# Optimization experiments

Measured on AMD Instinct MI355X. Metric: run time of the kernel, lower is better.

## Reference

```python
import jax, jax.numpy as jnp
import numpy as np

CORR_S = 8        # corr_size
IN_EPS = 1e-5     # torch InstanceNorm2d default eps
L2_EPS = 1e-12    # torch F.normalize default eps


def l2_normalize(x):
    # F.normalize(x, p=2, dim=1)
    n = jnp.sqrt(jnp.sum(x * x, axis=1, keepdims=True))
    return x / jnp.maximum(n, L2_EPS)


def instance_norm(x):
    # InstanceNorm2d(affine=False): per-sample, per-channel over H,W; biased var
    m = jnp.mean(x, axis=(2, 3), keepdims=True)
    v = jnp.var(x, axis=(2, 3), keepdims=True)
    return (x - m) * jax.lax.rsqrt(v + IN_EPS)


def setup_inputs() -> dict:
    key = jax.random.key(0)
    ks = jax.random.split(key, 7)
    B, C, H, W = 16, 256, 96, 96
    fc = 64                      # feat_channel
    p = CORR_S * CORR_S          # 64 correlation channels
    x = jax.random.normal(ks[0], (B, C, H, W), jnp.float32)
    # corr_reduce: Conv1x1(p->fc), IN, ReLU, Conv3x3(fc->fc)
    W1 = jax.random.normal(ks[1], (fc, p), jnp.float32) * 0.05
    b1 = jax.random.normal(ks[2], (fc,), jnp.float32) * 0.05
    W2 = jax.random.normal(ks[3], (fc, fc, 3, 3), jnp.float32) * 0.05
    b2 = jax.random.normal(ks[4], (fc,), jnp.float32) * 0.05
    # feat_adapt: Conv1x1(C+fc=320 -> fc), IN, ReLU
    W3 = jax.random.normal(ks[5], (fc, C + fc), jnp.float32) * 0.05
    b3 = jax.random.normal(ks[6], (fc,), jnp.float32) * 0.05
    return {"x": x, "W1": W1, "b1": b1, "W2": W2, "b2": b2, "W3": W3, "b3": b3}


def reference(x, W1, b1, W2, b2, W3, b3):
    B, C, H, W_ = x.shape
    s = CORR_S
    # AdaptiveAvgPool2d((s,s)): H,W divisible by s -> exact window means
    pooled = x.reshape(B, C, s, H // s, s, W_ // s).mean(axis=(3, 5))  # [B,C,s,s]
    ker = l2_normalize(pooled).reshape(B, C, s * s)  # [B,C,p]
    feat = l2_normalize(x)                            # [B,C,H,W]
    # corr_fun: per-sample 1x1 conv == batched contraction over channels
    corr = jnp.einsum('bcp,bchw->bphw', ker, feat)    # [B,p,H,W]
    # corr_reduce
    h = jnp.einsum('op,bphw->bohw', W1, corr) + b1[None, :, None, None]
    h = jax.nn.relu(instance_norm(h))
    h = jax.lax.conv_general_dilated(
        h, W2, window_strides=(1, 1), padding='SAME',
        dimension_numbers=('NCHW', 'OIHW', 'NCHW')) + b2[None, :, None, None]
    # feat_adapt on cat(x, Red_corr)
    new_feat = jnp.concatenate([x, h], axis=1)        # [B,C+fc,H,W]
    out = jnp.einsum('oc,bchw->bohw', W3, new_feat) + b3[None, :, None, None]
    out = jax.nn.relu(instance_norm(out))
    return out
```

## Files before the change

kernel.cpp:

```cpp
#include <hip/hip_runtime.h>

#define BB 16
#define CC 256
#define HW 9216

typedef short bf16x8 __attribute__((ext_vector_type(8)));
typedef float f32x4 __attribute__((ext_vector_type(4)));

__device__ __forceinline__ unsigned short f2bf(float f) {
  unsigned u = __float_as_uint(f);
  return (unsigned short)((u + 0x7FFFu + ((u >> 16) & 1u)) >> 16);
}
__device__ __forceinline__ float bf2f(unsigned short h) {
  return __uint_as_float(((unsigned)h) << 16);
}

__global__ __launch_bounds__(256) void k_pool(const float* __restrict__ x,
                                              float* __restrict__ pooled) {
  int bc = blockIdx.x;
  const float* plane = x + (size_t)bc * HW;
  __shared__ float rowwin[96][8];
  for (int idx = threadIdx.x; idx < 96 * 8; idx += 256) {
    int y = idx >> 3, wx = idx & 7;
    const float* r = plane + y * 96 + wx * 12;
    float s = 0.f;
#pragma unroll
    for (int i = 0; i < 12; ++i) s += r[i];
    rowwin[y][wx] = s;
  }
  __syncthreads();
  if (threadIdx.x < 64) {
    int wy = threadIdx.x >> 3, wx = threadIdx.x & 7;
    float s = 0.f;
#pragma unroll
    for (int i = 0; i < 12; ++i) s += rowwin[wy * 12 + i][wx];
    pooled[(size_t)bc * 64 + threadIdx.x] = s * (1.0f / 144.0f);
  }
}

__global__ __launch_bounds__(256) void k_invn(const float* __restrict__ pooled,
                                              float* __restrict__ invn) {
  int b = blockIdx.x;
  int p = threadIdx.x & 63, cg = threadIdx.x >> 6;
  const float* pb = pooled + (size_t)b * CC * 64;
  float s = 0.f;
  for (int c = cg; c < CC; c += 4) { float v = pb[c * 64 + p]; s += v * v; }
  __shared__ float sm[4][64];
  sm[cg][p] = s;
  __syncthreads();
  if (threadIdx.x < 64) {
    float tot = sm[0][p] + sm[1][p] + sm[2][p] + sm[3][p];
    invn[b * 64 + p] = 1.0f / fmaxf(sqrtf(tot), 1e-12f);
  }
}

__global__ __launch_bounds__(256) void k_M(const float* __restrict__ pooled,
                                           const float* __restrict__ invn,
                                           const float* __restrict__ W1,
                                           unsigned short* __restrict__ Mbf) {
  int c0 = blockIdx.x * 16, b = blockIdx.y, t = threadIdx.x;
  __shared__ float W1s[64][65];
  __shared__ float kers[16][65];
  __shared__ float invs[64];
  if (t < 64) invs[t] = invn[b * 64 + t];
  for (int i = t; i < 4096; i += 256) W1s[i >> 6][i & 63] = W1[i];
  __syncthreads();
  for (int i = t; i < 1024; i += 256) {
    int c = i >> 6, p = i & 63;
    kers[c][p] = pooled[((size_t)b * CC + c0 + c) * 64 + p] * invs[p];
  }
  __syncthreads();
  int c = t & 15, og = t >> 4;
  float s0 = 0.f, s1 = 0.f, s2 = 0.f, s3 = 0.f;
#pragma unroll
  for (int p = 0; p < 64; ++p) {
    float kv = kers[c][p];
    s0 = fmaf(W1s[og * 4 + 0][p], kv, s0);
    s1 = fmaf(W1s[og * 4 + 1][p], kv, s1);
    s2 = fmaf(W1s[og * 4 + 2][p], kv, s2);
    s3 = fmaf(W1s[og * 4 + 3][p], kv, s3);
  }
  unsigned short* Mb = Mbf + (size_t)b * 64 * 256 + c0 + c;
  Mb[(og * 4 + 0) * 256] = f2bf(s0);
  Mb[(og * 4 + 1) * 256] = f2bf(s1);
  Mb[(og * 4 + 2) * 256] = f2bf(s2);
  Mb[(og * 4 + 3) * 256] = f2bf(s3);
}

__global__ void k_prep(const float* __restrict__ W3, unsigned short* __restrict__ W3bf,
                       const float* __restrict__ W2, unsigned short* __restrict__ W2bf,
                       float* __restrict__ statsbuf) {
  int i = blockIdx.x * 256 + threadIdx.x;
  if (i < 64 * 320) W3bf[i] = f2bf(W3[i]);
  if (i < 9 * 64 * 64) {
    int tap = i >> 12, rem = i & 4095;
    int o = rem >> 6, f = rem & 63;
    W2bf[i] = f2bf(W2[(size_t)(o * 64 + f) * 9 + tap]);
  }
  if (i < 4096) statsbuf[i] = 0.f;
}

__global__ __launch_bounds__(256) void k_trans(const float* __restrict__ x,
                                               unsigned short* __restrict__ xT,
                                               float* __restrict__ ssq) {
  int b = blockIdx.y;
  int px0 = blockIdx.x * 64;
  int t = threadIdx.x;
  int px = t & 63, cg = t >> 6;
  __shared__ unsigned char sm[32768];
  __shared__ float sq[64];
  if (t < 64) sq[t] = 0.f;
  __syncthreads();
  float part = 0.f;
  const float* xb = x + (size_t)b * CC * HW + px0 + px;
#pragma unroll
  for (int kk = 0; kk < 8; ++kk) {
    int c = cg * 64 + kk * 8;
    float v[8];
#pragma unroll
    for (int j = 0; j < 8; ++j) {
      v[j] = xb[(size_t)(c + j) * HW];
      part += v[j] * v[j];
    }
    uint4 pk;
    pk.x = (unsigned)f2bf(v[0]) | ((unsigned)f2bf(v[1]) << 16);
    pk.y = (unsigned)f2bf(v[2]) | ((unsigned)f2bf(v[3]) << 16);
    pk.z = (unsigned)f2bf(v[4]) | ((unsigned)f2bf(v[5]) << 16);
    pk.w = (unsigned)f2bf(v[6]) | ((unsigned)f2bf(v[7]) << 16);
    int u = cg * 8 + kk;
    *(uint4*)(sm + px * 512 + ((u ^ (px & 31)) << 4)) = pk;
  }
  atomicAdd(&sq[px], part);
  __syncthreads();
  uint4* dst = (uint4*)(xT + ((size_t)b * HW + px0) * 256);
  for (int i = t; i < 2048; i += 256) {
    int p = i >> 5, q = i & 31;
    dst[i] = *(const uint4*)(sm + p * 512 + ((q ^ (p & 31)) << 4));
  }
  if (t < 64) ssq[(size_t)b * HW + px0 + t] = sq[t];
}

__global__ __launch_bounds__(256) void k_gemm1(
    const unsigned short* __restrict__ xT,
    const unsigned short* __restrict__ Mbf,
    const float* __restrict__ ssq,
    const float* __restrict__ b1,
    unsigned short* __restrict__ hpix,
    float* __restrict__ stats1) {
  int tile = blockIdx.x, b = blockIdx.y, t = threadIdx.x;
  int w = t >> 6, lane = t & 63, l15 = lane & 15, l4 = lane >> 4;
  int pixbase = tile * 256;
  __shared__ unsigned char Alds[32768];
  __shared__ float sb[128];
  {
    const uint4* src = (const uint4*)(Mbf + (size_t)b * 64 * 256);
    for (int i = t; i < 2048; i += 256) {
      int o = i >> 5, u = i & 31;
      *(uint4*)(Alds + o * 512 + ((u ^ (o & 7)) << 4)) = src[i];
    }
  }
  if (t < 128) sb[t] = 0.f;
  __syncthreads();
  f32x4 acc[4][4];
#pragma unroll
  for (int mf = 0; mf < 4; ++mf)
#pragma unroll
    for (int nf = 0; nf < 4; ++nf) { f32x4 z = {0.f,0.f,0.f,0.f}; acc[mf][nf] = z; }
  const unsigned short* xrow = xT + ((size_t)b * HW + pixbase + w * 64) * 256;
#pragma unroll
  for (int kk = 0; kk < 8; ++kk) {
    bf16x8 afr[4], bfr[4];
    int u = kk * 4 + l4;
#pragma unroll
    for (int mf = 0; mf < 4; ++mf)
      afr[mf] = *(const bf16x8*)(Alds + (mf * 16 + l15) * 512 + ((u ^ (l15 & 7)) << 4));
#pragma unroll
    for (int nf = 0; nf < 4; ++nf)
      bfr[nf] = *(const bf16x8*)(xrow + (size_t)(nf * 16 + l15) * 256 + kk * 32 + l4 * 8);
#pragma unroll
    for (int mf = 0; mf < 4; ++mf)
#pragma unroll
      for (int nf = 0; nf < 4; ++nf)
        acc[mf][nf] = __builtin_amdgcn_mfma_f32_16x16x32_bf16(afr[mf], bfr[nf], acc[mf][nf], 0, 0, 0);
  }
  float invs[4];
  const float* ssqb = ssq + (size_t)b * HW + pixbase + w * 64;
#pragma unroll
  for (int nf = 0; nf < 4; ++nf)
    invs[nf] = 1.0f / fmaxf(sqrtf(ssqb[nf * 16 + l15]), 1e-12f);
  float b1v[4][4];
#pragma unroll
  for (int mf = 0; mf < 4; ++mf)
#pragma unroll
    for (int i = 0; i < 4; ++i) b1v[mf][i] = b1[mf * 16 + l4 * 4 + i];
  float s_acc[4][4], ss_acc[4][4];
#pragma unroll
  for (int mf = 0; mf < 4; ++mf)
#pragma unroll
    for (int i = 0; i < 4; ++i) { s_acc[mf][i] = 0.f; ss_acc[mf][i] = 0.f; }
  __syncthreads();
#pragma unroll
  for (int mf = 0; mf < 4; ++mf)
#pragma unroll
    for (int nf = 0; nf < 4; ++nf) {
      float hv[4];
#pragma unroll
      for (int i = 0; i < 4; ++i) {
        hv[i] = fmaf(acc[mf][nf][i], invs[nf], b1v[mf][i]);
        s_acc[mf][i] += hv[i];
        ss_acc[mf][i] += hv[i] * hv[i];
      }
      uint2 pk;
      pk.x = (unsigned)f2bf(hv[0]) | ((unsigned)f2bf(hv[1]) << 16);
      pk.y = (unsigned)f2bf(hv[2]) | ((unsigned)f2bf(hv[3]) << 16);
      int px = w * 64 + nf * 16 + l15;
      int v = mf * 4 + l4;
      *(uint2*)(Alds + px * 128 + ((v ^ ((px & 7) << 1)) << 3)) = pk;
    }
#pragma unroll
  for (int mf = 0; mf < 4; ++mf)
#pragma unroll
    for (int i = 0; i < 4; ++i) {
      float s = s_acc[mf][i], q = ss_acc[mf][i];
#pragma unroll
      for (int m = 1; m < 16; m <<= 1) {
        s += __shfl_xor(s, m);
        q += __shfl_xor(q, m);
      }
      if (l15 == 0) {
        int o = mf * 16 + l4 * 4 + i;
        atomicAdd(&sb[o * 2], s);
        atomicAdd(&sb[o * 2 + 1], q);
      }
    }
  __syncthreads();
  uint4* dst = (uint4*)(hpix + ((size_t)b * HW + pixbase) * 64);
  for (int i = t; i < 2048; i += 256) {
    int p = i >> 3, u16 = i & 7;
    dst[i] = *(const uint4*)(Alds + p * 128 + ((u16 ^ (p & 7)) << 4));
  }
  if (t < 64) {
    atomicAdd(&stats1[(b * 64 + t) * 2], sb[t * 2]);
    atomicAdd(&stats1[(b * 64 + t) * 2 + 1], sb[t * 2 + 1]);
  }
}

__global__ __launch_bounds__(256) void k_conv_mfma(
    const unsigned short* __restrict__ hpix,
    const float* __restrict__ stats1,
    const unsigned short* __restrict__ W2bf, const float* __restrict__ b2,
    unsigned short* __restrict__ hh) {
  int band = blockIdx.x;
  int b = blockIdx.y;
  int t = threadIdx.x;
  int w = t >> 6;
  int lane = t & 63;
  int l15 = lane & 15, l4 = lane >> 4;

  __shared__ unsigned char smem[49152];
  __shared__ float scs[64], shs[64];
  if (t < 64) {
    float S = stats1[(b * 64 + t) * 2], SS = stats1[(b * 64 + t) * 2 + 1];
    float mean = S * (1.0f / (float)HW);
    float var = SS * (1.0f / (float)HW) - mean * mean;
    float rstd = rsqrtf(var + 1e-5f);
    scs[t] = rstd;
    shs[t] = -mean * rstd;
  }

  f32x4 acc[4][6];
#pragma unroll
  for (int mf = 0; mf < 4; ++mf)
#pragma unroll
    for (int nf = 0; nf < 6; ++nf) { f32x4 z = {0.f,0.f,0.f,0.f}; acc[mf][nf] = z; }

  for (int f0 = 0; f0 < 64; f0 += 32) {
    __syncthreads();
    for (int idx = t; idx < 6 * 98 * 8; idx += 256) {
      int f4 = idx & 7;
      int v = idx >> 3;
      int xr = v % 98;
      int r = v / 98;
      int gy = band * 4 - 1 + r;
      int gx = xr - 1;
      unsigned pk0 = 0, pk1 = 0;
      if ((unsigned)gy < 96u && (unsigned)gx < 96u) {
        const ushort4 rv = *(const ushort4*)(hpix +
            ((size_t)((size_t)b * HW + gy * 96 + gx) * 64 + f0 + f4 * 4));
        int fb = f0 + f4 * 4;
        float v0 = fmaxf(0.f, fmaf(bf2f(rv.x), scs[fb],     shs[fb]));
        float v1 = fmaxf(0.f, fmaf(bf2f(rv.y), scs[fb + 1], shs[fb + 1]));
        float v2 = fmaxf(0.f, fmaf(bf2f(rv.z), scs[fb + 2], shs[fb + 2]));
        float v3 = fmaxf(0.f, fmaf(bf2f(rv.w), scs[fb + 3], shs[fb + 3]));
        pk0 = (unsigned)f2bf(v0) | ((unsigned)f2bf(v1) << 16);
        pk1 = (unsigned)f2bf(v2) | ((unsigned)f2bf(v3) << 16);
      }
      int g = f4 >> 1;
      int gs = g ^ ((xr >> 1) & 3);
      unsigned loff = (unsigned)((r * 98 + xr) * 64 + gs * 16 + (f4 & 1) * 8);
      *(uint2*)(smem + loff) = make_uint2(pk0, pk1);
    }
    __syncthreads();
#pragma unroll
    for (int dy = 0; dy < 3; ++dy) {
      int r = w + dy;
#pragma unroll
      for (int dx = 0; dx < 3; ++dx) {
        int tap = dy * 3 + dx;
        bf16x8 afr[4];
#pragma unroll
        for (int mf = 0; mf < 4; ++mf) {
          int o = mf * 16 + l15;
          afr[mf] = *(const bf16x8*)(W2bf + ((size_t)(tap * 64 + o) * 64 + f0 + l4 * 8));
        }
#pragma unroll
        for (int nf = 0; nf < 6; ++nf) {
          int xr = nf * 16 + l15 + dx;
          unsigned loff = (unsigned)((r * 98 + xr) * 64 + ((l4 ^ ((xr >> 1) & 3)) * 16));
          bf16x8 bfr = *(const bf16x8*)(smem + loff);
#pragma unroll
          for (int mf = 0; mf < 4; ++mf)
            acc[mf][nf] = __builtin_amdgcn_mfma_f32_16x16x32_bf16(
                afr[mf], bfr, acc[mf][nf], 0, 0, 0);
        }
      }
    }
  }
  float b2v[4][4];
#pragma unroll
  for (int mf = 0; mf < 4; ++mf)
#pragma unroll
    for (int i = 0; i < 4; ++i) b2v[mf][i] = b2[mf * 16 + l4 * 4 + i];
  __syncthreads();
#pragma unroll
  for (int mf = 0; mf < 4; ++mf)
#pragma unroll
    for (int nf = 0; nf < 6; ++nf) {
      int tpx = w * 96 + nf * 16 + l15;
      float h0 = acc[mf][nf][0] + b2v[mf][0];
      float h1 = acc[mf][nf][1] + b2v[mf][1];
      float h2 = acc[mf][nf][2] + b2v[mf][2];
      float h3 = acc[mf][nf][3] + b2v[mf][3];
      uint2 pk;
      pk.x = (unsigned)f2bf(h0) | ((unsigned)f2bf(h1) << 16);
      pk.y = (unsigned)f2bf(h2) | ((unsigned)f2bf(h3) << 16);
      int v = mf * 4 + l4;
      *(uint2*)(smem + tpx * 128 + ((v ^ ((tpx & 7) << 1)) << 3)) = pk;
    }
  __syncthreads();
  uint4* dst = (uint4*)(hh + ((size_t)b * HW + band * 384) * 64);
  for (int i = t; i < 3072; i += 256) {
    int p = i >> 3, u16 = i & 7;
    dst[i] = *(const uint4*)(smem + p * 128 + ((u16 ^ (p & 7)) << 4));
  }
}

__global__ __launch_bounds__(256) void k_gemm2(
    const unsigned short* __restrict__ xT,
    const unsigned short* __restrict__ hh,
    const unsigned short* __restrict__ W3bf,
    const float* __restrict__ b3,
    unsigned short* __restrict__ opre,
    float* __restrict__ stats2) {
  int tile = blockIdx.x, b = blockIdx.y, t = threadIdx.x;
  int w = t >> 6, lane = t & 63, l15 = lane & 15, l4 = lane >> 4;
  int pixbase = tile * 256;
  __shared__ unsigned char Alds[40960];
  __shared__ float sb[128];
  {
    const uint4* src = (const uint4*)W3bf;
    for (int i = t; i < 2560; i += 256) {
      int o = i / 40, u = i - o * 40;
      *(uint4*)(Alds + o * 640 + ((u ^ (o & 7)) << 4)) = src[i];
    }
  }
  if (t < 128) sb[t] = 0.f;
  __syncthreads();
  f32x4 acc[4][4];
#pragma unroll
  for (int mf = 0; mf < 4; ++mf)
#pragma unroll
    for (int nf = 0; nf < 4; ++nf) { f32x4 z = {0.f,0.f,0.f,0.f}; acc[mf][nf] = z; }
  const unsigned short* xrow = xT + ((size_t)b * HW + pixbase + w * 64) * 256;
  const unsigned short* hrow = hh + ((size_t)b * HW + pixbase + w * 64) * 64;
#pragma unroll
  for (int kk = 0; kk < 8; ++kk) {
    bf16x8 afr[4], bfr[4];
    int u = kk * 4 + l4;
#pragma unroll
    for (int mf = 0; mf < 4; ++mf)
      afr[mf] = *(const bf16x8*)(Alds + (mf * 16 + l15) * 640 + ((u ^ (l15 & 7)) << 4));
#pragma unroll
    for (int nf = 0; nf < 4; ++nf)
      bfr[nf] = *(const bf16x8*)(xrow + (size_t)(nf * 16 + l15) * 256 + kk * 32 + l4 * 8);
#pragma unroll
    for (int mf = 0; mf < 4; ++mf)
#pragma unroll
      for (int nf = 0; nf < 4; ++nf)
        acc[mf][nf] = __builtin_amdgcn_mfma_f32_16x16x32_bf16(afr[mf], bfr[nf], acc[mf][nf], 0, 0, 0);
  }
#pragma unroll
  for (int kk = 8; kk < 10; ++kk) {
    bf16x8 afr[4], bfr[4];
    int u = kk * 4 + l4;
#pragma unroll
    for (int mf = 0; mf < 4; ++mf)
      afr[mf] = *(const bf16x8*)(Alds + (mf * 16 + l15) * 640 + ((u ^ (l15 & 7)) << 4));
#pragma unroll
    for (int nf = 0; nf < 4; ++nf)
      bfr[nf] = *(const bf16x8*)(hrow + (size_t)(nf * 16 + l15) * 64 + (kk - 8) * 32 + l4 * 8);
#pragma unroll
    for (int mf = 0; mf < 4; ++mf)
#pragma unroll
      for (int nf = 0; nf < 4; ++nf)
        acc[mf][nf] = __builtin_amdgcn_mfma_f32_16x16x32_bf16(afr[mf], bfr[nf], acc[mf][nf], 0, 0, 0);
  }
  float b3v[4][4];
#pragma unroll
  for (int mf = 0; mf < 4; ++mf)
#pragma unroll
    for (int i = 0; i < 4; ++i) b3v[mf][i] = b3[mf * 16 + l4 * 4 + i];
  float s_acc[4][4], ss_acc[4][4];
#pragma unroll
  for (int mf = 0; mf < 4; ++mf)
#pragma unroll
    for (int i = 0; i < 4; ++i) { s_acc[mf][i] = 0.f; ss_acc[mf][i] = 0.f; }
  __syncthreads();
#pragma unroll
  for (int mf = 0; mf < 4; ++mf)
#pragma unroll
    for (int nf = 0; nf < 4; ++nf) {
      float hv[4];
#pragma unroll
      for (int i = 0; i < 4; ++i) {
        hv[i] = acc[mf][nf][i] + b3v[mf][i];
        s_acc[mf][i] += hv[i];
        ss_acc[mf][i] += hv[i] * hv[i];
      }
      uint2 pk;
      pk.x = (unsigned)f2bf(hv[0]) | ((unsigned)f2bf(hv[1]) << 16);
      pk.y = (unsigned)f2bf(hv[2]) | ((unsigned)f2bf(hv[3]) << 16);
      int px = w * 64 + nf * 16 + l15;
      int v = mf * 4 + l4;
      *(uint2*)(Alds + px * 128 + ((v ^ ((px & 7) << 1)) << 3)) = pk;
    }
#pragma unroll
  for (int mf = 0; mf < 4; ++mf)
#pragma unroll
    for (int i = 0; i < 4; ++i) {
      float s = s_acc[mf][i], q = ss_acc[mf][i];
#pragma unroll
      for (int m = 1; m < 16; m <<= 1) {
        s += __shfl_xor(s, m);
        q += __shfl_xor(q, m);
      }
      if (l15 == 0) {
        int o = mf * 16 + l4 * 4 + i;
        atomicAdd(&sb[o * 2], s);
        atomicAdd(&sb[o * 2 + 1], q);
      }
    }
  __syncthreads();
  uint4* dst = (uint4*)(opre + ((size_t)b * HW + pixbase) * 64);
  for (int i = t; i < 2048; i += 256) {
    int p = i >> 3, u16 = i & 7;
    dst[i] = *(const uint4*)(Alds + p * 128 + ((u16 ^ (p & 7)) << 4));
  }
  if (t < 64) {
    atomicAdd(&stats2[(b * 64 + t) * 2], sb[t * 2]);
    atomicAdd(&stats2[(b * 64 + t) * 2 + 1], sb[t * 2 + 1]);
  }
}

__global__ __launch_bounds__(256) void k_apply(const unsigned short* __restrict__ opre,
                                               const float* __restrict__ stats2,
                                               float* __restrict__ out) {
  int b = blockIdx.y, px0 = blockIdx.x * 64, t = threadIdx.x;
  __shared__ float tile[64][68];
  __shared__ float scs[64], shs[64];
  if (t < 64) {
    float S = stats2[(b * 64 + t) * 2], SS = stats2[(b * 64 + t) * 2 + 1];
    float mean = S * (1.0f / (float)HW);
    float var = SS * (1.0f / (float)HW) - mean * mean;
    float rstd = rsqrtf(var + 1e-5f);
    scs[t] = rstd;
    shs[t] = -mean * rstd;
  }
  __syncthreads();
  const unsigned* src = (const unsigned*)(opre + ((size_t)b * HW + px0) * 64);
  for (int i = t; i < 2048; i += 256) {
    int px = i >> 5, q = i & 31;
    unsigned v = src[i];
    int o = q * 2;
    float f0 = bf2f((unsigned short)(v & 0xffff));
    float f1 = bf2f((unsigned short)(v >> 16));
    tile[o][px]     = fmaxf(0.f, fmaf(f0, scs[o], shs[o]));
    tile[o + 1][px] = fmaxf(0.f, fmaf(f1, scs[o + 1], shs[o + 1]));
  }
  __syncthreads();
  for (int j = t; j < 1024; j += 256) {
    int o = j >> 4, w4 = j & 15;
    float4 v = *(const float4*)(&tile[o][w4 * 4]);
    *(float4*)(out + ((size_t)(b * 64) + o) * HW + px0 + w4 * 4) = v;
  }
}

extern "C" void kernel_launch(void* const* d_in, const int* in_sizes, int n_in,
                              void* d_out, int out_size, void* d_ws, size_t ws_size,
                              hipStream_t stream) {
  const float* x  = (const float*)d_in[0];
  const float* W1 = (const float*)d_in[1];
  const float* b1 = (const float*)d_in[2];
  const float* W2 = (const float*)d_in[3];
  const float* b2 = (const float*)d_in[4];
  const float* W3 = (const float*)d_in[5];
  const float* b3 = (const float*)d_in[6];
  float* out = (float*)d_out;

  float* ws = (float*)d_ws;
  float* pooled = ws;
  float* invn   = ws + 262144;
  float* ssq    = ws + 263168;
  float* stats  = ws + 414720;
  float* stats1 = stats;
  float* stats2 = stats + 2048;
  unsigned short* Mbf  = (unsigned short*)(ws + 418816);
  unsigned short* W3bf = (unsigned short*)(ws + 549888);
  unsigned short* W2bf = (unsigned short*)(ws + 560128);
  unsigned short* hpix = (unsigned short*)(ws + 578560);
  unsigned short* xT   = (unsigned short*)(ws + 5297152);
  unsigned short* hh   = (unsigned short*)d_out;
  unsigned short* opre = hpix;

  k_prep<<<dim3(144), dim3(256), 0, stream>>>(W3, W3bf, W2, W2bf, stats);
  k_pool<<<dim3(BB * CC), dim3(256), 0, stream>>>(x, pooled);
  k_invn<<<dim3(BB), dim3(256), 0, stream>>>(pooled, invn);
  k_M<<<dim3(16, BB), dim3(256), 0, stream>>>(pooled, invn, W1, Mbf);
  k_trans<<<dim3(144, BB), dim3(256), 0, stream>>>(x, xT, ssq);
  k_gemm1<<<dim3(36, BB), dim3(256), 0, stream>>>(xT, Mbf, ssq, b1, hpix, stats1);
  k_conv_mfma<<<dim3(24, BB), dim3(256), 0, stream>>>(hpix, stats1, W2bf, b2, hh);
  k_gemm2<<<dim3(36, BB), dim3(256), 0, stream>>>(xT, hh, W3bf, b3, opre, stats2);
  k_apply<<<dim3(144, BB), dim3(256), 0, stream>>>(opre, stats2, out);
}
```

Measured before the change: 215.9 us.

## Fuse adaptive average pooling into the transpose kernel with atomic window sums

Drops the standalone pooling kernel, which made a full extra pass over the fp32 input. Instead, the transpose kernel sums its staged bf16 tile per channel and per 12x12 window and atomically adds the result into a pooled buffer that the prep kernel now zeroes. Pooled values become unscaled sums, which is harmless because the L2 normalization cancels the scale. In exchange it adds a serial 64-step LDS loop per thread, global atomics, and pooling done from bf16-rounded values instead of fp32.

```diff
diff --git a/kernel.cpp b/kernel.cpp
--- a/kernel.cpp
+++ b/kernel.cpp
@@ -13,29 +13,6 @@
 }
 __device__ __forceinline__ float bf2f(unsigned short h) {
   return __uint_as_float(((unsigned)h) << 16);
-}
-
-__global__ __launch_bounds__(256) void k_pool(const float* __restrict__ x,
-                                              float* __restrict__ pooled) {
-  int bc = blockIdx.x;
-  const float* plane = x + (size_t)bc * HW;
-  __shared__ float rowwin[96][8];
-  for (int idx = threadIdx.x; idx < 96 * 8; idx += 256) {
-    int y = idx >> 3, wx = idx & 7;
-    const float* r = plane + y * 96 + wx * 12;
-    float s = 0.f;
-#pragma unroll
-    for (int i = 0; i < 12; ++i) s += r[i];
-    rowwin[y][wx] = s;
-  }
-  __syncthreads();
-  if (threadIdx.x < 64) {
-    int wy = threadIdx.x >> 3, wx = threadIdx.x & 7;
-    float s = 0.f;
-#pragma unroll
-    for (int i = 0; i < 12; ++i) s += rowwin[wy * 12 + i][wx];
-    pooled[(size_t)bc * 64 + threadIdx.x] = s * (1.0f / 144.0f);
-  }
 }
 
 __global__ __launch_bounds__(256) void k_invn(const float* __restrict__ pooled,
@@ -89,7 +66,7 @@
 
 __global__ void k_prep(const float* __restrict__ W3, unsigned short* __restrict__ W3bf,
                        const float* __restrict__ W2, unsigned short* __restrict__ W2bf,
-                       float* __restrict__ statsbuf) {
+                       float* __restrict__ statsbuf, float* __restrict__ pooled) {
   int i = blockIdx.x * 256 + threadIdx.x;
   if (i < 64 * 320) W3bf[i] = f2bf(W3[i]);
   if (i < 9 * 64 * 64) {
@@ -98,11 +75,13 @@
     W2bf[i] = f2bf(W2[(size_t)(o * 64 + f) * 9 + tap]);
   }
   if (i < 4096) statsbuf[i] = 0.f;
+  for (int j = i; j < BB * CC * 64; j += 144 * 256) pooled[j] = 0.f;
 }
 
 __global__ __launch_bounds__(256) void k_trans(const float* __restrict__ x,
                                                unsigned short* __restrict__ xT,
-                                               float* __restrict__ ssq) {
+                                               float* __restrict__ ssq,
+                                               float* __restrict__ pooled) {
   int b = blockIdx.y;
   int px0 = blockIdx.x * 64;
   int t = threadIdx.x;
@@ -138,6 +117,30 @@
     dst[i] = *(const uint4*)(sm + p * 512 + ((q ^ (p & 31)) << 4));
   }
   if (t < 64) ssq[(size_t)b * HW + px0 + t] = sq[t];
+  {
+    int c = t;
+    int ubase = (c >> 3) & 31;
+    int boff = (c & 7) * 2;
+    size_t pbase = ((size_t)b * CC + c) * 64;
+    int y = px0 / 96;
+    int xcol = px0 - y * 96;
+    int curw = (y / 12) * 8 + xcol / 12;
+    float run = 0.f;
+#pragma unroll 4
+    for (int i = 0; i < 64; ++i) {
+      float v = bf2f(*(const unsigned short*)(sm + i * 512 + ((ubase ^ (i & 31)) << 4) + boff));
+      run += v;
+      ++xcol;
+      if (xcol == 96) { xcol = 0; ++y; }
+      int nw = (y / 12) * 8 + xcol / 12;
+      if (nw != curw && i != 63) {
+        atomicAdd(&pooled[pbase + curw], run);
+        run = 0.f;
+        curw = nw;
+      }
+    }
+    atomicAdd(&pooled[pbase + curw], run);
+  }
 }
 
 __global__ __launch_bounds__(256) void k_gemm1(
@@ -532,11 +535,10 @@
   unsigned short* hh   = (unsigned short*)d_out;
   unsigned short* opre = hpix;
 
-  k_prep<<<dim3(144), dim3(256), 0, stream>>>(W3, W3bf, W2, W2bf, stats);
-  k_pool<<<dim3(BB * CC), dim3(256), 0, stream>>>(x, pooled);
+  k_prep<<<dim3(144), dim3(256), 0, stream>>>(W3, W3bf, W2, W2bf, stats, pooled);
+  k_trans<<<dim3(144, BB), dim3(256), 0, stream>>>(x, xT, ssq, pooled);
   k_invn<<<dim3(BB), dim3(256), 0, stream>>>(pooled, invn);
   k_M<<<dim3(16, BB), dim3(256), 0, stream>>>(pooled, invn, W1, Mbf);
-  k_trans<<<dim3(144, BB), dim3(256), 0, stream>>>(x, xT, ssq);
   k_gemm1<<<dim3(36, BB), dim3(256), 0, stream>>>(xT, Mbf, ssq, b1, hpix, stats1);
   k_conv_mfma<<<dim3(24, BB), dim3(256), 0, stream>>>(hpix, stats1, W2bf, b2, hh);
   k_gemm2<<<dim3(36, BB), dim3(256), 0, stream>>>(xT, hh, W3bf, b3, opre, stats2);
```

Result: slower. 336.6 us (+55.9%).

## Fuse transpose with both GEMMs and fold W3 x-part into conv kernel

Applied to the files above, without the earlier changes.

The x transpose kernel now also runs the correlation GEMM and the x-part of the feat_adapt GEMM directly from shared memory. This removes the bf16 xT round trip and the separate gemm1 kernel. The partial result y0 is stored as fp32 in channel-major layout. The conv kernel then adds the W3 contribution of the conv output and computes the second statistics, which removes the gemm2 kernel and the hh buffer. The cost is an fp32 y0 buffer (16x64x9216 floats) that is written and read back, plus per-block global atomics on stats1 from many more blocks.

```diff
diff --git a/kernel.cpp b/kernel.cpp
--- a/kernel.cpp
+++ b/kernel.cpp
@@ -100,13 +100,19 @@
   if (i < 4096) statsbuf[i] = 0.f;
 }
 
-__global__ __launch_bounds__(256) void k_trans(const float* __restrict__ x,
-                                               unsigned short* __restrict__ xT,
-                                               float* __restrict__ ssq) {
+__global__ __launch_bounds__(256) void k_tg1(
+    const float* __restrict__ x,
+    const unsigned short* __restrict__ Mbf,
+    const unsigned short* __restrict__ W3bf,
+    const float* __restrict__ b1,
+    unsigned short* __restrict__ hpix,
+    float* __restrict__ y0,
+    float* __restrict__ stats1) {
   int b = blockIdx.y;
   int px0 = blockIdx.x * 64;
   int t = threadIdx.x;
   int px = t & 63, cg = t >> 6;
+  int w = t >> 6, lane = t & 63, l15 = lane & 15, l4 = lane >> 4;
   __shared__ unsigned char sm[32768];
   __shared__ float sq[64];
   if (t < 64) sq[t] = 0.f;
@@ -132,124 +138,86 @@
   }
   atomicAdd(&sq[px], part);
   __syncthreads();
-  uint4* dst = (uint4*)(xT + ((size_t)b * HW + px0) * 256);
-  for (int i = t; i < 2048; i += 256) {
-    int p = i >> 5, q = i & 31;
-    dst[i] = *(const uint4*)(sm + p * 512 + ((q ^ (p & 31)) << 4));
-  }
-  if (t < 64) ssq[(size_t)b * HW + px0 + t] = sq[t];
-}
-
-__global__ __launch_bounds__(256) void k_gemm1(
-    const unsigned short* __restrict__ xT,
-    const unsigned short* __restrict__ Mbf,
-    const float* __restrict__ ssq,
-    const float* __restrict__ b1,
-    unsigned short* __restrict__ hpix,
-    float* __restrict__ stats1) {
-  int tile = blockIdx.x, b = blockIdx.y, t = threadIdx.x;
-  int w = t >> 6, lane = t & 63, l15 = lane & 15, l4 = lane >> 4;
-  int pixbase = tile * 256;
-  __shared__ unsigned char Alds[32768];
-  __shared__ float sb[128];
-  {
-    const uint4* src = (const uint4*)(Mbf + (size_t)b * 64 * 256);
-    for (int i = t; i < 2048; i += 256) {
-      int o = i >> 5, u = i & 31;
-      *(uint4*)(Alds + o * 512 + ((u ^ (o & 7)) << 4)) = src[i];
-    }
-  }
-  if (t < 128) sb[t] = 0.f;
-  __syncthreads();
-  f32x4 acc[4][4];
-#pragma unroll
-  for (int mf = 0; mf < 4; ++mf)
-#pragma unroll
-    for (int nf = 0; nf < 4; ++nf) { f32x4 z = {0.f,0.f,0.f,0.f}; acc[mf][nf] = z; }
-  const unsigned short* xrow = xT + ((size_t)b * HW + pixbase + w * 64) * 256;
+  f32x4 acch[4], accy[4];
+#pragma unroll
+  for (int nf = 0; nf < 4; ++nf) { f32x4 z = {0.f,0.f,0.f,0.f}; acch[nf] = z; accy[nf] = z; }
+  const unsigned short* Ma = Mbf + ((size_t)b * 64 + w * 16 + l15) * 256;
+  const unsigned short* Wa = W3bf + (size_t)(w * 16 + l15) * 320;
 #pragma unroll
   for (int kk = 0; kk < 8; ++kk) {
-    bf16x8 afr[4], bfr[4];
+    bf16x8 am = *(const bf16x8*)(Ma + kk * 32 + l4 * 8);
+    bf16x8 aw = *(const bf16x8*)(Wa + kk * 32 + l4 * 8);
     int u = kk * 4 + l4;
 #pragma unroll
-    for (int mf = 0; mf < 4; ++mf)
-      afr[mf] = *(const bf16x8*)(Alds + (mf * 16 + l15) * 512 + ((u ^ (l15 & 7)) << 4));
-#pragma unroll
-    for (int nf = 0; nf < 4; ++nf)
-      bfr[nf] = *(const bf16x8*)(xrow + (size_t)(nf * 16 + l15) * 256 + kk * 32 + l4 * 8);
-#pragma unroll
-    for (int mf = 0; mf < 4; ++mf)
-#pragma unroll
-      for (int nf = 0; nf < 4; ++nf)
-        acc[mf][nf] = __builtin_amdgcn_mfma_f32_16x16x32_bf16(afr[mf], bfr[nf], acc[mf][nf], 0, 0, 0);
-  }
-  float invs[4];
-  const float* ssqb = ssq + (size_t)b * HW + pixbase + w * 64;
+    for (int nf = 0; nf < 4; ++nf) {
+      int p2 = nf * 16 + l15;
+      bf16x8 bfr = *(const bf16x8*)(sm + p2 * 512 + ((u ^ (p2 & 31)) << 4));
+      acch[nf] = __builtin_amdgcn_mfma_f32_16x16x32_bf16(am, bfr, acch[nf], 0, 0, 0);
+      accy[nf] = __builtin_amdgcn_mfma_f32_16x16x32_bf16(aw, bfr, accy[nf], 0, 0, 0);
+    }
+  }
+  float inv[4];
 #pragma unroll
   for (int nf = 0; nf < 4; ++nf)
-    invs[nf] = 1.0f / fmaxf(sqrtf(ssqb[nf * 16 + l15]), 1e-12f);
-  float b1v[4][4];
-#pragma unroll
-  for (int mf = 0; mf < 4; ++mf)
-#pragma unroll
-    for (int i = 0; i < 4; ++i) b1v[mf][i] = b1[mf * 16 + l4 * 4 + i];
-  float s_acc[4][4], ss_acc[4][4];
-#pragma unroll
-  for (int mf = 0; mf < 4; ++mf)
-#pragma unroll
-    for (int i = 0; i < 4; ++i) { s_acc[mf][i] = 0.f; ss_acc[mf][i] = 0.f; }
-  __syncthreads();
-#pragma unroll
-  for (int mf = 0; mf < 4; ++mf)
-#pragma unroll
-    for (int nf = 0; nf < 4; ++nf) {
-      float hv[4];
-#pragma unroll
-      for (int i = 0; i < 4; ++i) {
-        hv[i] = fmaf(acc[mf][nf][i], invs[nf], b1v[mf][i]);
-        s_acc[mf][i] += hv[i];
-        ss_acc[mf][i] += hv[i] * hv[i];
-      }
-      uint2 pk;
-      pk.x = (unsigned)f2bf(hv[0]) | ((unsigned)f2bf(hv[1]) << 16);
-      pk.y = (unsigned)f2bf(hv[2]) | ((unsigned)f2bf(hv[3]) << 16);
-      int px = w * 64 + nf * 16 + l15;
-      int v = mf * 4 + l4;
-      *(uint2*)(Alds + px * 128 + ((v ^ ((px & 7) << 1)) << 3)) = pk;
-    }
-#pragma unroll
-  for (int mf = 0; mf < 4; ++mf)
+    inv[nf] = 1.0f / fmaxf(sqrtf(sq[nf * 16 + l15]), 1e-12f);
+  float b1v[4];
+#pragma unroll
+  for (int i = 0; i < 4; ++i) b1v[i] = b1[w * 16 + l4 * 4 + i];
+  float s_acc[4], ss_acc[4];
+#pragma unroll
+  for (int i = 0; i < 4; ++i) { s_acc[i] = 0.f; ss_acc[i] = 0.f; }
+  __syncthreads();
+#pragma unroll
+  for (int nf = 0; nf < 4; ++nf) {
+    float hv[4];
 #pragma unroll
     for (int i = 0; i < 4; ++i) {
-      float s = s_acc[mf][i], q = ss_acc[mf][i];
-#pragma unroll
-      for (int m = 1; m < 16; m <<= 1) {
-        s += __shfl_xor(s, m);
-        q += __shfl_xor(q, m);
-      }
-      if (l15 == 0) {
-        int o = mf * 16 + l4 * 4 + i;
-        atomicAdd(&sb[o * 2], s);
-        atomicAdd(&sb[o * 2 + 1], q);
-      }
-    }
-  __syncthreads();
-  uint4* dst = (uint4*)(hpix + ((size_t)b * HW + pixbase) * 64);
-  for (int i = t; i < 2048; i += 256) {
+      hv[i] = fmaf(acch[nf][i], inv[nf], b1v[i]);
+      s_acc[i] += hv[i];
+      ss_acc[i] += hv[i] * hv[i];
+    }
+    uint2 pk;
+    pk.x = (unsigned)f2bf(hv[0]) | ((unsigned)f2bf(hv[1]) << 16);
+    pk.y = (unsigned)f2bf(hv[2]) | ((unsigned)f2bf(hv[3]) << 16);
+    int p2 = nf * 16 + l15;
+    int v = w * 4 + l4;
+    *(uint2*)(sm + p2 * 128 + ((v ^ ((p2 & 7) << 1)) << 3)) = pk;
+#pragma unroll
+    for (int i = 0; i < 4; ++i)
+      y0[((size_t)(b * 64 + w * 16 + l4 * 4 + i)) * HW + px0 + nf * 16 + l15] = accy[nf][i];
+  }
+#pragma unroll
+  for (int i = 0; i < 4; ++i) {
+    float s = s_acc[i], q = ss_acc[i];
+#pragma unroll
+    for (int m = 1; m < 16; m <<= 1) {
+      s += __shfl_xor(s, m);
+      q += __shfl_xor(q, m);
+    }
+    if (l15 == 0) {
+      int o = w * 16 + l4 * 4 + i;
+      atomicAdd(&stats1[(b * 64 + o) * 2], s);
+      atomicAdd(&stats1[(b * 64 + o) * 2 + 1], q);
+    }
+  }
+  __syncthreads();
+  uint4* dst = (uint4*)(hpix + ((size_t)b * HW + px0) * 64);
+  for (int i = t; i < 512; i += 256) {
     int p = i >> 3, u16 = i & 7;
-    dst[i] = *(const uint4*)(Alds + p * 128 + ((u16 ^ (p & 7)) << 4));
-  }
-  if (t < 64) {
-    atomicAdd(&stats1[(b * 64 + t) * 2], sb[t * 2]);
-    atomicAdd(&stats1[(b * 64 + t) * 2 + 1], sb[t * 2 + 1]);
-  }
-}
-
-__global__ __launch_bounds__(256) void k_conv_mfma(
+    dst[i] = *(const uint4*)(sm + p * 128 + ((u16 ^ (p & 7)) << 4));
+  }
+}
+
+__global__ __launch_bounds__(256) void k_cg2(
     const unsigned short* __restrict__ hpix,
     const float* __restrict__ stats1,
-    const unsigned short* __restrict__ W2bf, const float* __restrict__ b2,
-    unsigned short* __restrict__ hh) {
+    const unsigned short* __restrict__ W2bf,
+    const float* __restrict__ b2,
+    const float* __restrict__ y0,
+    const unsigned short* __restrict__ W3bf,
+    const float* __restrict__ b3,
+    unsigned short* __restrict__ opre,
+    float* __restrict__ stats2) {
   int band = blockIdx.x;
   int b = blockIdx.y;
   int t = threadIdx.x;
@@ -348,127 +316,95 @@
       *(uint2*)(smem + tpx * 128 + ((v ^ ((tpx & 7) << 1)) << 3)) = pk;
     }
   __syncthreads();
-  uint4* dst = (uint4*)(hh + ((size_t)b * HW + band * 384) * 64);
+  f32x4 acc2[4][6];
+  {
+    const size_t pxg = (size_t)b * HW + band * 384 + (size_t)w * 96;
+#pragma unroll
+    for (int mf = 0; mf < 4; ++mf)
+#pragma unroll
+      for (int i = 0; i < 4; ++i) {
+        int o = mf * 16 + l4 * 4 + i;
+        const float* yrow = y0 + ((size_t)b * 64 + o) * HW + band * 384 + w * 96 + l15;
+#pragma unroll
+        for (int nf = 0; nf < 6; ++nf) acc2[mf][nf][i] = yrow[nf * 16];
+      }
+    (void)pxg;
+  }
+#pragma unroll
+  for (int kk = 0; kk < 2; ++kk) {
+    bf16x8 afr[4];
+#pragma unroll
+    for (int mf = 0; mf < 4; ++mf)
+      afr[mf] = *(const bf16x8*)(W3bf + (size_t)(mf * 16 + l15) * 320 + 256 + kk * 32 + l4 * 8);
+#pragma unroll
+    for (int nf = 0; nf < 6; ++nf) {
+      int tpx = w * 96 + nf * 16 + l15;
+      int v0 = kk * 8 + l4 * 2;
+      union { bf16x8 v; uint2 h[2]; } bb;
+      bb.h[0] = *(const uint2*)(smem + tpx * 128 + (((v0    ) ^ ((tpx & 7) << 1)) << 3));
+      bb.h[1] = *(const uint2*)(smem + tpx * 128 + (((v0 + 1) ^ ((tpx & 7) << 1)) << 3));
+#pragma unroll
+      for (int mf = 0; mf < 4; ++mf)
+        acc2[mf][nf] = __builtin_amdgcn_mfma_f32_16x16x32_bf16(afr[mf], bb.v, acc2[mf][nf], 0, 0, 0);
+    }
+  }
+  float b3v[4][4];
+#pragma unroll
+  for (int mf = 0; mf < 4; ++mf)
+#pragma unroll
+    for (int i = 0; i < 4; ++i) b3v[mf][i] = b3[mf * 16 + l4 * 4 + i];
+  float s_acc[4][4], ss_acc[4][4];
+#pragma unroll
+  for (int mf = 0; mf < 4; ++mf)
+#pragma unroll
+    for (int i = 0; i < 4; ++i) { s_acc[mf][i] = 0.f; ss_acc[mf][i] = 0.f; }
+#pragma unroll
+  for (int mf = 0; mf < 4; ++mf)
+#pragma unroll
+    for (int nf = 0; nf < 6; ++nf)
+#pragma unroll
+      for (int i = 0; i < 4; ++i) {
+        float hv = acc2[mf][nf][i] + b3v[mf][i];
+        s_acc[mf][i] += hv;
+        ss_acc[mf][i] += hv * hv;
+      }
+#pragma unroll
+  for (int mf = 0; mf < 4; ++mf)
+#pragma unroll
+    for (int i = 0; i < 4; ++i) {
+      float s = s_acc[mf][i], q = ss_acc[mf][i];
+#pragma unroll
+      for (int m = 1; m < 16; m <<= 1) {
+        s += __shfl_xor(s, m);
+        q += __shfl_xor(q, m);
+      }
+      if (l15 == 0) {
+        int o = mf * 16 + l4 * 4 + i;
+        atomicAdd(&stats2[(b * 64 + o) * 2], s);
+        atomicAdd(&stats2[(b * 64 + o) * 2 + 1], q);
+      }
+    }
+  __syncthreads();
+#pragma unroll
+  for (int mf = 0; mf < 4; ++mf)
+#pragma unroll
+    for (int nf = 0; nf < 6; ++nf) {
+      int tpx = w * 96 + nf * 16 + l15;
+      float h0 = acc2[mf][nf][0] + b3v[mf][0];
+      float h1 = acc2[mf][nf][1] + b3v[mf][1];
+      float h2 = acc2[mf][nf][2] + b3v[mf][2];
+      float h3 = acc2[mf][nf][3] + b3v[mf][3];
+      uint2 pk;
+      pk.x = (unsigned)f2bf(h0) | ((unsigned)f2bf(h1) << 16);
+      pk.y = (unsigned)f2bf(h2) | ((unsigned)f2bf(h3) << 16);
+      int v = mf * 4 + l4;
+      *(uint2*)(smem + tpx * 128 + ((v ^ ((tpx & 7) << 1)) << 3)) = pk;
+    }
+  __syncthreads();
+  uint4* dst = (uint4*)(opre + ((size_t)b * HW + band * 384) * 64);
   for (int i = t; i < 3072; i += 256) {
     int p = i >> 3, u16 = i & 7;
     dst[i] = *(const uint4*)(smem + p * 128 + ((u16 ^ (p & 7)) << 4));
-  }
-}
-
-__global__ __launch_bounds__(256) void k_gemm2(
-    const unsigned short* __restrict__ xT,
-    const unsigned short* __restrict__ hh,
-    const unsigned short* __restrict__ W3bf,
-    const float* __restrict__ b3,
-    unsigned short* __restrict__ opre,
-    float* __restrict__ stats2) {
-  int tile = blockIdx.x, b = blockIdx.y, t = threadIdx.x;
-  int w = t >> 6, lane = t & 63, l15 = lane & 15, l4 = lane >> 4;
-  int pixbase = tile * 256;
-  __shared__ unsigned char Alds[40960];
-  __shared__ float sb[128];
-  {
-    const uint4* src = (const uint4*)W3bf;
-    for (int i = t; i < 2560; i += 256) {
-      int o = i / 40, u = i - o * 40;
-      *(uint4*)(Alds + o * 640 + ((u ^ (o & 7)) << 4)) = src[i];
-    }
-  }
-  if (t < 128) sb[t] = 0.f;
-  __syncthreads();
-  f32x4 acc[4][4];
-#pragma unroll
-  for (int mf = 0; mf < 4; ++mf)
-#pragma unroll
-    for (int nf = 0; nf < 4; ++nf) { f32x4 z = {0.f,0.f,0.f,0.f}; acc[mf][nf] = z; }
-  const unsigned short* xrow = xT + ((size_t)b * HW + pixbase + w * 64) * 256;
-  const unsigned short* hrow = hh + ((size_t)b * HW + pixbase + w * 64) * 64;
-#pragma unroll
-  for (int kk = 0; kk < 8; ++kk) {
-    bf16x8 afr[4], bfr[4];
-    int u = kk * 4 + l4;
-#pragma unroll
-    for (int mf = 0; mf < 4; ++mf)
-      afr[mf] = *(const bf16x8*)(Alds + (mf * 16 + l15) * 640 + ((u ^ (l15 & 7)) << 4));
-#pragma unroll
-    for (int nf = 0; nf < 4; ++nf)
-      bfr[nf] = *(const bf16x8*)(xrow + (size_t)(nf * 16 + l15) * 256 + kk * 32 + l4 * 8);
-#pragma unroll
-    for (int mf = 0; mf < 4; ++mf)
-#pragma unroll
-      for (int nf = 0; nf < 4; ++nf)
-        acc[mf][nf] = __builtin_amdgcn_mfma_f32_16x16x32_bf16(afr[mf], bfr[nf], acc[mf][nf], 0, 0, 0);
-  }
-#pragma unroll
-  for (int kk = 8; kk < 10; ++kk) {
-    bf16x8 afr[4], bfr[4];
-    int u = kk * 4 + l4;
-#pragma unroll
-    for (int mf = 0; mf < 4; ++mf)
-      afr[mf] = *(const bf16x8*)(Alds + (mf * 16 + l15) * 640 + ((u ^ (l15 & 7)) << 4));
-#pragma unroll
-    for (int nf = 0; nf < 4; ++nf)
-      bfr[nf] = *(const bf16x8*)(hrow + (size_t)(nf * 16 + l15) * 64 + (kk - 8) * 32 + l4 * 8);
-#pragma unroll
-    for (int mf = 0; mf < 4; ++mf)
-#pragma unroll
-      for (int nf = 0; nf < 4; ++nf)
-        acc[mf][nf] = __builtin_amdgcn_mfma_f32_16x16x32_bf16(afr[mf], bfr[nf], acc[mf][nf], 0, 0, 0);
-  }
-  float b3v[4][4];
-#pragma unroll
-  for (int mf = 0; mf < 4; ++mf)
-#pragma unroll
-    for (int i = 0; i < 4; ++i) b3v[mf][i] = b3[mf * 16 + l4 * 4 + i];
-  float s_acc[4][4], ss_acc[4][4];
-#pragma unroll
-  for (int mf = 0; mf < 4; ++mf)
-#pragma unroll
-    for (int i = 0; i < 4; ++i) { s_acc[mf][i] = 0.f; ss_acc[mf][i] = 0.f; }
-  __syncthreads();
-#pragma unroll
-  for (int mf = 0; mf < 4; ++mf)
-#pragma unroll
-    for (int nf = 0; nf < 4; ++nf) {
-      float hv[4];
-#pragma unroll
-      for (int i = 0; i < 4; ++i) {
-        hv[i] = acc[mf][nf][i] + b3v[mf][i];
-        s_acc[mf][i] += hv[i];
-        ss_acc[mf][i] += hv[i] * hv[i];
-      }
-      uint2 pk;
-      pk.x = (unsigned)f2bf(hv[0]) | ((unsigned)f2bf(hv[1]) << 16);
-      pk.y = (unsigned)f2bf(hv[2]) | ((unsigned)f2bf(hv[3]) << 16);
-      int px = w * 64 + nf * 16 + l15;
-      int v = mf * 4 + l4;
-      *(uint2*)(Alds + px * 128 + ((v ^ ((px & 7) << 1)) << 3)) = pk;
-    }
-#pragma unroll
-  for (int mf = 0; mf < 4; ++mf)
-#pragma unroll
-    for (int i = 0; i < 4; ++i) {
-      float s = s_acc[mf][i], q = ss_acc[mf][i];
-#pragma unroll
-      for (int m = 1; m < 16; m <<= 1) {
-        s += __shfl_xor(s, m);
-        q += __shfl_xor(q, m);
-      }
-      if (l15 == 0) {
-        int o = mf * 16 + l4 * 4 + i;
-        atomicAdd(&sb[o * 2], s);
-        atomicAdd(&sb[o * 2 + 1], q);
-      }
-    }
-  __syncthreads();
-  uint4* dst = (uint4*)(opre + ((size_t)b * HW + pixbase) * 64);
-  for (int i = t; i < 2048; i += 256) {
-    int p = i >> 3, u16 = i & 7;
-    dst[i] = *(const uint4*)(Alds + p * 128 + ((u16 ^ (p & 7)) << 4));
-  }
-  if (t < 64) {
-    atomicAdd(&stats2[(b * 64 + t) * 2], sb[t * 2]);
-    atomicAdd(&stats2[(b * 64 + t) * 2 + 1], sb[t * 2 + 1]);
   }
 }
 
@@ -520,25 +456,21 @@
   float* ws = (float*)d_ws;
   float* pooled = ws;
   float* invn   = ws + 262144;
-  float* ssq    = ws + 263168;
-  float* stats  = ws + 414720;
+  float* stats  = ws + 263168;
   float* stats1 = stats;
   float* stats2 = stats + 2048;
-  unsigned short* Mbf  = (unsigned short*)(ws + 418816);
-  unsigned short* W3bf = (unsigned short*)(ws + 549888);
-  unsigned short* W2bf = (unsigned short*)(ws + 560128);
-  unsigned short* hpix = (unsigned short*)(ws + 578560);
-  unsigned short* xT   = (unsigned short*)(ws + 5297152);
-  unsigned short* hh   = (unsigned short*)d_out;
-  unsigned short* opre = hpix;
+  unsigned short* Mbf  = (unsigned short*)(ws + 267264);
+  unsigned short* W3bf = (unsigned short*)(ws + 398336);
+  unsigned short* W2bf = (unsigned short*)(ws + 408576);
+  unsigned short* hpix = (unsigned short*)(ws + 427008);
+  float* y0            = ws + 5145600;
+  unsigned short* opre = (unsigned short*)(ws + 14582784);
 
   k_prep<<<dim3(144), dim3(256), 0, stream>>>(W3, W3bf, W2, W2bf, stats);
   k_pool<<<dim3(BB * CC), dim3(256), 0, stream>>>(x, pooled);
   k_invn<<<dim3(BB), dim3(256), 0, stream>>>(pooled, invn);
   k_M<<<dim3(16, BB), dim3(256), 0, stream>>>(pooled, invn, W1, Mbf);
-  k_trans<<<dim3(144, BB), dim3(256), 0, stream>>>(x, xT, ssq);
-  k_gemm1<<<dim3(36, BB), dim3(256), 0, stream>>>(xT, Mbf, ssq, b1, hpix, stats1);
-  k_conv_mfma<<<dim3(24, BB), dim3(256), 0, stream>>>(hpix, stats1, W2bf, b2, hh);
-  k_gemm2<<<dim3(36, BB), dim3(256), 0, stream>>>(xT, hh, W3bf, b3, opre, stats2);
+  k_tg1<<<dim3(144, BB), dim3(256), 0, stream>>>(x, Mbf, W3bf, b1, hpix, y0, stats1);
+  k_cg2<<<dim3(24, BB), dim3(256), 0, stream>>>(hpix, stats1, W2bf, b2, y0, W3bf, b3, opre, stats2);
   k_apply<<<dim3(144, BB), dim3(256), 0, stream>>>(opre, stats2, out);
 }
```

Result: slower. 265.3 us (+22.9%).
